# Optimization experiments

Hardware: AMD Instinct MI355X
Metric: run time of the kernel (lower is better)

The kernel has to match this reference:

```python
import jax, jax.numpy as jnp
import numpy as np

E = 100000          # number of edges
NS, NV = 128, 64    # scalar / vector multiplicities of node irreps (128x0e + 64x1e)
FC = 64             # radial MLP width (fc_neurons = [64, 64])
WN = NS + NS + NV + NV + NV   # depthwise-TP weight numel = 448
VOUT = 64           # gated vector channels after linear
EPS = 1e-5
SQRT3 = 3.0 ** 0.5
SQRT2 = 2.0 ** 0.5


def setup_inputs() -> dict:
    key = jax.random.key(0)
    ks = jax.random.split(key, 12)

    def n(k, shape, scale=1.0):
        return jax.random.normal(k, shape, dtype=jnp.float32) * scale

    return dict(
        node_input=n(ks[0], (E, NS + 3 * NV)),   # [E, 320] gathered node features
        edge_attr=n(ks[1], (E, 4)),              # [E, 1(0e) + 3(1e)] spherical harmonics
        edge_scalars=n(ks[2], (E, FC)),          # [E, 64] radial embedding
        # radial MLP (RadialProfile): 64 -> 64 -> 64 -> 448 (+ offset)
        W1=n(ks[3], (FC, FC), FC ** -0.5), b1=jnp.zeros((FC,), jnp.float32),
        W2=n(ks[4], (FC, FC), FC ** -0.5), b2=jnp.zeros((FC,), jnp.float32),
        W3=n(ks[5], (FC, WN), FC ** -0.5), offset=jnp.zeros((WN,), jnp.float32),
        # irrep-wise linear (LinearRS): scalars 192->192 (incl. gates), vectors 256->64
        Ws=n(ks[6], (NS + NV, NS + NV), (NS + NV) ** -0.5),
        bs=jnp.zeros((NS + NV,), jnp.float32),
        Wv=n(ks[7], (NS + 2 * NV, VOUT), (NS + 2 * NV) ** -0.5),
        # equivariant layer-norm affine params
        g_s=jnp.ones((NS + NV,), jnp.float32), b_n=jnp.zeros((NS + NV,), jnp.float32),
        g_v=jnp.ones((VOUT,), jnp.float32),
    )


def _forward(node_input, edge_attr, edge_scalars, W1, b1, W2, b2, W3, offset,
             Ws, bs, Wv, g_s, b_n, g_v):
    # --- radial MLP -> per-edge depthwise-TP weights (dtp_rad) ---
    h = jax.nn.silu(edge_scalars @ W1 + b1)
    h = jax.nn.silu(h @ W2 + b2)
    w = h @ W3 + offset                                   # [E, 448]
    w1 = w[:, :NS]                 # 0e x 0e -> 0e  (128)
    w2 = w[:, NS:2 * NS]           # 0e x 1e -> 1e  (128)
    w3 = w[:, 2 * NS:2 * NS + NV]  # 1e x 0e -> 1e  (64)
    w4 = w[:, 2 * NS + NV:2 * NS + 2 * NV]   # 1e x 1e -> 0e (64)
    w5 = w[:, 2 * NS + 2 * NV:]              # 1e x 1e -> 1e (64)

    s = node_input[:, :NS]                    # [E, 128] scalar block
    v = node_input[:, NS:].reshape(-1, NV, 3) # [E, 64, 3] vector block
    e0 = edge_attr[:, 0:1]                    # [E, 1]
    e1 = edge_attr[:, 1:4]                    # [E, 3]

    # --- depthwise tensor product (per-edge CG contractions, 'uvu') ---
    o0a = w1 * s * e0                                          # [E,128]
    o0b = w4 * (v * e1[:, None, :]).sum(-1) / SQRT3            # [E,64]
    o1a = (w2 * s)[:, :, None] * e1[:, None, :]                # [E,128,3]
    o1b = w3[:, :, None] * v * e0[:, :, None]                  # [E,64,3]
    o1c = w5[:, :, None] * jnp.cross(v, e1[:, None, :]) / SQRT2  # [E,64,3]

    scal = jnp.concatenate([o0a, o0b], axis=-1)                # [E,192]
    vec = jnp.concatenate([o1a, o1b, o1c], axis=1)             # [E,256,3]

    # --- irrep-wise linear mix ---
    s_lin = scal @ Ws + bs                                     # [E,192]
    v_lin = jnp.einsum('euc,uo->eoc', vec, Wv)                 # [E,64,3]

    # --- equivariant layer norm (component normalization per irrep block) ---
    s_c = s_lin - s_lin.mean(-1, keepdims=True)
    s_norm = jax.lax.rsqrt((s_c ** 2).mean(-1, keepdims=True) + EPS)
    s_n = g_s * s_c * s_norm + b_n
    v_norm = jax.lax.rsqrt((v_lin ** 2).sum(-1).mean(-1) + EPS)  # [E]
    v_n = g_v[:, None] * v_lin * v_norm[:, None, None]

    # --- gated activation: SiLU on scalars, sigmoid gates on vectors ---
    out_s = jax.nn.silu(s_n[:, :NS])                           # [E,128]
    gates = jax.nn.sigmoid(s_n[:, NS:])                        # [E,64]
    out_v = v_n * gates[:, :, None]                            # [E,64,3]
    return jnp.concatenate([out_s, out_v.reshape(-1, 3 * VOUT)], axis=-1)


def reference(node_input, edge_attr, edge_scalars, W1, b1, W2, b2, W3, offset,
              Ws, bs, Wv, g_s, b_n, g_v):
    return _forward(node_input, edge_attr, edge_scalars, W1, b1, W2, b2, W3, offset,
                    Ws, bs, Wv, g_s, b_n, g_v)
```

## Files before the change

### kernel.cpp

```cpp
#include <hip/hip_runtime.h>

typedef short short8 __attribute__((ext_vector_type(8)));
typedef __bf16 bf16x8 __attribute__((ext_vector_type(8)));
typedef float f32x4 __attribute__((ext_vector_type(4)));

namespace {

constexpr int kNodeW = 320;
constexpr int kOutW  = 320;

constexpr int F_W1 = 0;
constexpr int F_W2 = 8;
constexpr int F_W3 = 16;
constexpr int F_WS = 72;
constexpr int F_WP = 144;
constexpr int F_WQ = 160;
constexpr int F_WR = 168;
constexpr int NFRAG = 176;

constexpr int WAVES = 4;
constexpr int ARENA_OFF = 152 * 1024;
constexpr int SMEM_SZ = 160 * 1024;

constexpr float RS3 = 0.5773502691896258f;
constexpr float RS2 = 0.7071067811865476f;

__device__ __forceinline__ ushort f2b(float f) {
  __bf16 b = (__bf16)f;
  return __builtin_bit_cast(ushort, b);
}
__device__ __forceinline__ float fsig(float x) { return 1.0f / (1.0f + __expf(-x)); }
__device__ __forceinline__ float fsilu(float x) { return x / (1.0f + __expf(-x)); }
__device__ __forceinline__ f32x4 MFMA(short8 a, short8 b, f32x4 c) {
  return __builtin_amdgcn_mfma_f32_16x16x32_bf16(
      __builtin_bit_cast(bf16x8, a), __builtin_bit_cast(bf16x8, b), c, 0, 0, 0);
}

__device__ __forceinline__ void cw16(char* ar, int row, int col, ushort v) {
  *(ushort*)(ar + ((row * 128 + col * 2) ^ ((row & 7) << 4))) = v;
}
__device__ __forceinline__ short8 cra(const char* ar, int row, int kb, int lg) {
  return *(const short8*)(ar + ((row * 128 + kb * 64 + lg * 16) ^ ((row & 7) << 4)));
}

__global__ void pack_weights(const float* __restrict__ W1, const float* __restrict__ W2,
                             const float* __restrict__ W3, const float* __restrict__ Ws,
                             const float* __restrict__ Wv, ushort* __restrict__ dst) {
  int f = blockIdx.x, lane = threadIdx.x;
  const float* src; int ldw, kbase, NT, local;
  if (f < 8)        { src = W1; ldw = 64;  kbase = 0;   NT = 4;  local = f; }
  else if (f < 16)  { src = W2; ldw = 64;  kbase = 0;   NT = 4;  local = f - 8; }
  else if (f < 72)  { src = W3; ldw = 448; kbase = 0;   NT = 28; local = f - 16; }
  else if (f < 144) { src = Ws; ldw = 192; kbase = 0;   NT = 12; local = f - 72; }
  else if (f < 160) { src = Wv; ldw = 64;  kbase = 0;   NT = 4;  local = f - 144; }
  else if (f < 168) { src = Wv; ldw = 64;  kbase = 128; NT = 4;  local = f - 160; }
  else              { src = Wv; ldw = 64;  kbase = 192; NT = 4;  local = f - 168; }
  int kb = local / NT, nt = local % NT;
  int k0  = kbase + kb * 32 + (lane >> 4) * 8;
  int col = nt * 16 + (lane & 15);
  ushort* o = dst + ((size_t)f * 64 + lane) * 8;
#pragma unroll
  for (int j = 0; j < 8; ++j) o[j] = f2b(src[(size_t)(k0 + j) * ldw + col]);
}

__global__ __launch_bounds__(256, 1) void fctp_main(
    const float* __restrict__ node, const float* __restrict__ eattr,
    const float* __restrict__ es, const float* __restrict__ b1,
    const float* __restrict__ b2, const float* __restrict__ offs,
    const float* __restrict__ bs, const float* __restrict__ g_s,
    const float* __restrict__ b_n, const float* __restrict__ g_v,
    const short8* __restrict__ wsv, float* __restrict__ out, int E) {
  __shared__ __align__(16) char smem[SMEM_SZ];
  const int lane = threadIdx.x & 63, wave = threadIdx.x >> 6;
  const int l15 = lane & 15, lg = lane >> 4;

#pragma unroll
  for (int i = 0; i < 38; ++i) {
    int fl = wave * 38 + i;
    int fg = (fl < 56)  ? (F_W3 + fl)
           : (fl < 128) ? (F_WS + (fl - 56))
           : (fl < 136) ? (F_WQ + (fl - 128))
           : (fl < 144) ? (F_WR + (fl - 136))
                        : (F_WP + (fl - 144));
    *(short8*)(smem + fl * 1024 + lane * 16) = wsv[fg * 64 + lane];
  }
  __syncthreads();

  short8 w1f[8], w2f[8];
#pragma unroll
  for (int i = 0; i < 8; ++i) {
    w1f[i] = wsv[(F_W1 + i) * 64 + lane];
    w2f[i] = wsv[(F_W2 + i) * 64 + lane];
  }

  char* ar = smem + ARENA_OFF + wave * 2048;
  auto ldsB = [&](int f) -> short8 {
    return *(const short8*)(smem + f * 1024 + lane * 16);
  };

  const int ntiles = (E + 15) >> 4;
  for (int tile = (int)blockIdx.x * WAVES + wave; tile < ntiles;
       tile += (int)gridDim.x * WAVES) {
    const int e0 = tile * 16;
    int geA = e0 + l15; if (geA >= E) geA = E - 1;
    int geR[4];
    float e0v[4], e1v[4][3];
#pragma unroll
    for (int r = 0; r < 4; ++r) {
      int g = e0 + lg * 4 + r; if (g >= E) g = E - 1;
      geR[r] = g;
      float4 ea = *(const float4*)(eattr + (size_t)g * 4);
      e0v[r] = ea.x; e1v[r][0] = ea.y; e1v[r][1] = ea.z; e1v[r][2] = ea.w;
    }

    float sn[4][8];
    float vn[4][4][3];
#pragma unroll
    for (int r = 0; r < 4; ++r) {
      const float* ni = node + (size_t)geR[r] * kNodeW;
#pragma unroll
      for (int nt = 0; nt < 8; ++nt) sn[r][nt] = ni[nt * 16 + l15];
#pragma unroll
      for (int nt = 0; nt < 4; ++nt) {
        const float* vp = ni + 128 + 3 * (nt * 16 + l15);
        vn[r][nt][0] = vp[0]; vn[r][nt][1] = vp[1]; vn[r][nt][2] = vp[2];
      }
    }

    short8 aes[2];
#pragma unroll
    for (int kb = 0; kb < 2; ++kb) {
      const float* p = es + (size_t)geA * 64 + kb * 32 + lg * 8;
      float4 xa = *(const float4*)p, xb = *(const float4*)(p + 4);
      short8 a;
      a[0] = (short)f2b(xa.x); a[1] = (short)f2b(xa.y); a[2] = (short)f2b(xa.z); a[3] = (short)f2b(xa.w);
      a[4] = (short)f2b(xb.x); a[5] = (short)f2b(xb.y); a[6] = (short)f2b(xb.z); a[7] = (short)f2b(xb.w);
      aes[kb] = a;
    }

    short8 ah[2];
    {
      f32x4 acc[4];
#pragma unroll
      for (int nt = 0; nt < 4; ++nt) { float bv = b1[nt * 16 + l15]; acc[nt] = (f32x4){bv, bv, bv, bv}; }
      __builtin_amdgcn_s_setprio(1);
#pragma unroll
      for (int kb = 0; kb < 2; ++kb)
#pragma unroll
        for (int nt = 0; nt < 4; ++nt)
          acc[nt] = MFMA(aes[kb], w1f[kb * 4 + nt], acc[nt]);
      __builtin_amdgcn_s_setprio(0);
#pragma unroll
      for (int nt = 0; nt < 4; ++nt)
#pragma unroll
        for (int r = 0; r < 4; ++r)
          cw16(ar, lg * 4 + r, nt * 16 + l15, f2b(fsilu(acc[nt][r])));
      ah[0] = cra(ar, l15, 0, lg);
      ah[1] = cra(ar, l15, 1, lg);
    }
    {
      f32x4 acc[4];
#pragma unroll
      for (int nt = 0; nt < 4; ++nt) { float bv = b2[nt * 16 + l15]; acc[nt] = (f32x4){bv, bv, bv, bv}; }
      __builtin_amdgcn_s_setprio(1);
#pragma unroll
      for (int kb = 0; kb < 2; ++kb)
#pragma unroll
        for (int nt = 0; nt < 4; ++nt)
          acc[nt] = MFMA(ah[kb], w2f[kb * 4 + nt], acc[nt]);
      __builtin_amdgcn_s_setprio(0);
#pragma unroll
      for (int nt = 0; nt < 4; ++nt)
#pragma unroll
        for (int r = 0; r < 4; ++r)
          cw16(ar, lg * 4 + r, nt * 16 + l15, f2b(fsilu(acc[nt][r])));
      ah[0] = cra(ar, l15, 0, lg);
      ah[1] = cra(ar, l15, 1, lg);
    }

    auto wseg = [&](int seg, f32x4 (&w)[4]) {
#pragma unroll
      for (int nt = 0; nt < 4; ++nt) {
        float bv = offs[seg * 64 + nt * 16 + l15];
        w[nt] = (f32x4){bv, bv, bv, bv};
      }
      __builtin_amdgcn_s_setprio(1);
#pragma unroll
      for (int kb = 0; kb < 2; ++kb)
#pragma unroll
        for (int nt = 0; nt < 4; ++nt)
          w[nt] = MFMA(ah[kb], ldsB(kb * 28 + seg * 4 + nt), w[nt]);
      __builtin_amdgcn_s_setprio(0);
    };
    auto gemm12 = [&](int kb0, f32x4 (&sac)[12]) {
      short8 a0 = cra(ar, l15, 0, lg), a1 = cra(ar, l15, 1, lg);
      __builtin_amdgcn_s_setprio(1);
#pragma unroll
      for (int nt = 0; nt < 12; ++nt)
        sac[nt] = MFMA(a0, ldsB(56 + kb0 * 12 + nt), sac[nt]);
#pragma unroll
      for (int nt = 0; nt < 12; ++nt)
        sac[nt] = MFMA(a1, ldsB(56 + (kb0 + 1) * 12 + nt), sac[nt]);
      __builtin_amdgcn_s_setprio(0);
    };
    auto gemm4g = [&](int fb0, int fb1, f32x4 (&ac)[4]) {
      short8 a0 = cra(ar, l15, 0, lg), a1 = cra(ar, l15, 1, lg);
      __builtin_amdgcn_s_setprio(1);
#pragma unroll
      for (int nt = 0; nt < 4; ++nt) ac[nt] = MFMA(a0, wsv[(fb0 + nt) * 64 + lane], ac[nt]);
#pragma unroll
      for (int nt = 0; nt < 4; ++nt) ac[nt] = MFMA(a1, wsv[(fb1 + nt) * 64 + lane], ac[nt]);
      __builtin_amdgcn_s_setprio(0);
    };
    auto gemm4L = [&](int s0, f32x4 (&ac)[4]) {
      short8 a0 = cra(ar, l15, 0, lg), a1 = cra(ar, l15, 1, lg);
      __builtin_amdgcn_s_setprio(1);
#pragma unroll
      for (int nt = 0; nt < 4; ++nt) ac[nt] = MFMA(a0, ldsB(s0 + nt), ac[nt]);
#pragma unroll
      for (int nt = 0; nt < 4; ++nt) ac[nt] = MFMA(a1, ldsB(s0 + 4 + nt), ac[nt]);
      __builtin_amdgcn_s_setprio(0);
    };
    auto tpS = [&](const f32x4 (&w)[4], int nb, bool mulE0) {
#pragma unroll
      for (int nt = 0; nt < 4; ++nt)
#pragma unroll
        for (int r = 0; r < 4; ++r) {
          float v = w[nt][r] * sn[r][nb + nt];
          if (mulE0) v *= e0v[r];
          cw16(ar, lg * 4 + r, nt * 16 + l15, f2b(v));
        }
    };
    auto tpD = [&](const f32x4 (&w)[4]) {
#pragma unroll
      for (int nt = 0; nt < 4; ++nt)
#pragma unroll
        for (int r = 0; r < 4; ++r) {
          float dot = vn[r][nt][0] * e1v[r][0] + vn[r][nt][1] * e1v[r][1] +
                      vn[r][nt][2] * e1v[r][2];
          cw16(ar, lg * 4 + r, nt * 16 + l15, f2b(w[nt][r] * dot * RS3));
        }
    };
    auto tpQ = [&](const f32x4 (&w)[4], int c) {
#pragma unroll
      for (int nt = 0; nt < 4; ++nt)
#pragma unroll
        for (int r = 0; r < 4; ++r)
          cw16(ar, lg * 4 + r, nt * 16 + l15,
               f2b(e0v[r] * w[nt][r] * vn[r][nt][c]));
    };
    auto tpR = [&](const f32x4 (&w)[4], int c) {
      const int i1 = (c + 1) % 3, i2 = (c + 2) % 3;
#pragma unroll
      for (int nt = 0; nt < 4; ++nt)
#pragma unroll
        for (int r = 0; r < 4; ++r) {
          float cr = vn[r][nt][i1] * e1v[r][i2] - vn[r][nt][i2] * e1v[r][i1];
          cw16(ar, lg * 4 + r, nt * 16 + l15, f2b(w[nt][r] * cr * RS2));
        }
    };

    f32x4 wacc[4];
    f32x4 sacc[12];
#pragma unroll
    for (int nt = 0; nt < 12; ++nt) { float bv = bs[nt * 16 + l15]; sacc[nt] = (f32x4){bv, bv, bv, bv}; }
    wseg(0, wacc); tpS(wacc, 0, true);  gemm12(0, sacc);
    wseg(1, wacc); tpS(wacc, 4, true);  gemm12(2, sacc);
    wseg(5, wacc); tpD(wacc);           gemm12(4, sacc);

    float gate[4][4];
    {
      float gsv[12], bnv[12];
#pragma unroll
      for (int nt = 0; nt < 12; ++nt) { gsv[nt] = g_s[nt * 16 + l15]; bnv[nt] = b_n[nt * 16 + l15]; }
#pragma unroll
      for (int r = 0; r < 4; ++r) {
        float sx = 0.f, sxx = 0.f;
#pragma unroll
        for (int nt = 0; nt < 12; ++nt) { float v = sacc[nt][r]; sx += v; sxx += v * v; }
#pragma unroll
        for (int m = 8; m >= 1; m >>= 1) { sx += __shfl_xor(sx, m); sxx += __shfl_xor(sxx, m); }
        float mean = sx * (1.0f / 192.0f);
        float var  = sxx * (1.0f / 192.0f) - mean * mean;
        float rstd = rsqrtf(var + 1e-5f);
        int geu = e0 + lg * 4 + r;
        bool valid = geu < E;
        float* ob = out + (size_t)(valid ? geu : 0) * kOutW;
#pragma unroll
        for (int nt = 0; nt < 12; ++nt) {
          float s_n = gsv[nt] * (sacc[nt][r] - mean) * rstd + bnv[nt];
          if (nt < 8) { if (valid) ob[nt * 16 + l15] = fsilu(s_n); }
          else gate[r][nt - 8] = fsig(s_n);
        }
      }
    }

    f32x4 pacc[4];
#pragma unroll
    for (int nt = 0; nt < 4; ++nt) pacc[nt] = (f32x4){0.f, 0.f, 0.f, 0.f};
    wseg(2, wacc); tpS(wacc, 0, false); gemm4L(144, pacc);
    wseg(3, wacc); tpS(wacc, 4, false); gemm4g(F_WP + 8, F_WP + 12, pacc);

    f32x4 vl[3][4];
    wseg(4, wacc);
#pragma unroll
    for (int c = 0; c < 3; ++c) {
#pragma unroll
      for (int nt = 0; nt < 4; ++nt)
#pragma unroll
        for (int r = 0; r < 4; ++r)
          vl[c][nt][r] = pacc[nt][r] * e1v[r][c];
      tpQ(wacc, c);
      gemm4L(128, vl[c]);
    }
    wseg(6, wacc);
#pragma unroll
    for (int c = 0; c < 3; ++c) {
      tpR(wacc, c);
      gemm4L(136, vl[c]);
    }

    {
      float gvv[4];
#pragma unroll
      for (int nt = 0; nt < 4; ++nt) gvv[nt] = g_v[nt * 16 + l15];
#pragma unroll
      for (int r = 0; r < 4; ++r) {
        float vsq = 0.f;
#pragma unroll
        for (int c = 0; c < 3; ++c)
#pragma unroll
          for (int nt = 0; nt < 4; ++nt) { float v = vl[c][nt][r]; vsq += v * v; }
#pragma unroll
        for (int m = 8; m >= 1; m >>= 1) vsq += __shfl_xor(vsq, m);
        float vnrm = rsqrtf(vsq * (1.0f / 64.0f) + 1e-5f);
        int geu = e0 + lg * 4 + r;
        if (geu < E) {
          float* ob = out + (size_t)geu * kOutW + 128;
#pragma unroll
          for (int nt = 0; nt < 4; ++nt) {
            float m3 = gvv[nt] * vnrm * gate[r][nt];
            int o3 = (nt * 16 + l15) * 3;
            ob[o3 + 0] = m3 * vl[0][nt][r];
            ob[o3 + 1] = m3 * vl[1][nt][r];
            ob[o3 + 2] = m3 * vl[2][nt][r];
          }
        }
      }
    }
  }
}

}

extern "C" void kernel_launch(void* const* d_in, const int* in_sizes, int n_in,
                              void* d_out, int out_size, void* d_ws, size_t ws_size,
                              hipStream_t stream) {
  const float* node_input   = (const float*)d_in[0];
  const float* edge_attr    = (const float*)d_in[1];
  const float* edge_scalars = (const float*)d_in[2];
  const float* W1 = (const float*)d_in[3];
  const float* b1 = (const float*)d_in[4];
  const float* W2 = (const float*)d_in[5];
  const float* b2 = (const float*)d_in[6];
  const float* W3 = (const float*)d_in[7];
  const float* offset = (const float*)d_in[8];
  const float* Ws = (const float*)d_in[9];
  const float* bs = (const float*)d_in[10];
  const float* Wv = (const float*)d_in[11];
  const float* g_s = (const float*)d_in[12];
  const float* b_n = (const float*)d_in[13];
  const float* g_v = (const float*)d_in[14];
  float* out = (float*)d_out;

  const int E = in_sizes[0] / kNodeW;

  pack_weights<<<NFRAG, 64, 0, stream>>>(W1, W2, W3, Ws, Wv, (ushort*)d_ws);

  const int ntiles = (E + 15) / 16;
  int blocks = (ntiles + WAVES - 1) / WAVES;
  if (blocks > 256) blocks = 256;
  fctp_main<<<blocks, WAVES * 64, 0, stream>>>(
      node_input, edge_attr, edge_scalars, b1, b2, offset, bs, g_s, b_n, g_v,
      (const short8*)d_ws, out, E);
}
```

Measured before the change: 180.0 us.

## Software-pipeline per-tile global loads with double-buffered register state

Restructures the persistent tile loop so each wave prefetches the next tile's edge attributes, scalar node features, edge scalars and vector node features into a second register state while the current tile's GEMMs run. The loop is unrolled by two and alternates between two EState buffers. The aim is to hide global-memory latency behind MFMA work. In exchange it roughly doubles the per-thread register footprint for input state, which risks spills or lower occupancy. Prefetch addresses past the end are clamped to E-1, so those reads stay in bounds.

```diff
diff --git a/kernel.cpp b/kernel.cpp
--- a/kernel.cpp
+++ b/kernel.cpp
@@ -42,6 +42,15 @@
 __device__ __forceinline__ short8 cra(const char* ar, int row, int kb, int lg) {
   return *(const short8*)(ar + ((row * 128 + kb * 64 + lg * 16) ^ ((row & 7) << 4)));
 }
+
+struct EState {
+  int   geR[4];
+  float e0v[4];
+  float e1v[4][3];
+  float sn[4][8];
+  float vn[4][4][3];
+  float4 esr[4];
+};
 
 __global__ void pack_weights(const float* __restrict__ W1, const float* __restrict__ W2,
                              const float* __restrict__ W3, const float* __restrict__ Ws,
@@ -99,39 +108,52 @@
   };
 
   const int ntiles = (E + 15) >> 4;
-  for (int tile = (int)blockIdx.x * WAVES + wave; tile < ntiles;
-       tile += (int)gridDim.x * WAVES) {
-    const int e0 = tile * 16;
+  const int stride = (int)gridDim.x * WAVES;
+  int tl0 = (int)blockIdx.x * WAVES + wave;
+  if (tl0 >= ntiles) return;
+
+  auto loadHead = [&](int tl, EState& S) {
+    const int e0 = tl * 16;
     int geA = e0 + l15; if (geA >= E) geA = E - 1;
-    int geR[4];
-    float e0v[4], e1v[4][3];
 #pragma unroll
     for (int r = 0; r < 4; ++r) {
       int g = e0 + lg * 4 + r; if (g >= E) g = E - 1;
-      geR[r] = g;
+      S.geR[r] = g;
       float4 ea = *(const float4*)(eattr + (size_t)g * 4);
-      e0v[r] = ea.x; e1v[r][0] = ea.y; e1v[r][1] = ea.z; e1v[r][2] = ea.w;
-    }
-
-    float sn[4][8];
-    float vn[4][4][3];
+      S.e0v[r] = ea.x; S.e1v[r][0] = ea.y; S.e1v[r][1] = ea.z; S.e1v[r][2] = ea.w;
+    }
 #pragma unroll
     for (int r = 0; r < 4; ++r) {
-      const float* ni = node + (size_t)geR[r] * kNodeW;
-#pragma unroll
-      for (int nt = 0; nt < 8; ++nt) sn[r][nt] = ni[nt * 16 + l15];
+      const float* ni = node + (size_t)S.geR[r] * kNodeW;
+#pragma unroll
+      for (int nt = 0; nt < 8; ++nt) S.sn[r][nt] = ni[nt * 16 + l15];
+    }
+#pragma unroll
+    for (int kb = 0; kb < 2; ++kb) {
+      const float* p = es + (size_t)geA * 64 + kb * 32 + lg * 8;
+      S.esr[kb * 2]     = *(const float4*)p;
+      S.esr[kb * 2 + 1] = *(const float4*)(p + 4);
+    }
+  };
+  auto loadVn = [&](EState& S) {
+#pragma unroll
+    for (int r = 0; r < 4; ++r) {
+      const float* ni = node + (size_t)S.geR[r] * kNodeW;
 #pragma unroll
       for (int nt = 0; nt < 4; ++nt) {
         const float* vp = ni + 128 + 3 * (nt * 16 + l15);
-        vn[r][nt][0] = vp[0]; vn[r][nt][1] = vp[1]; vn[r][nt][2] = vp[2];
+        S.vn[r][nt][0] = vp[0]; S.vn[r][nt][1] = vp[1]; S.vn[r][nt][2] = vp[2];
       }
     }
+  };
+
+  auto body = [&](int tl, EState& C, EState& N) {
+    const int e0 = tl * 16;
 
     short8 aes[2];
 #pragma unroll
     for (int kb = 0; kb < 2; ++kb) {
-      const float* p = es + (size_t)geA * 64 + kb * 32 + lg * 8;
-      float4 xa = *(const float4*)p, xb = *(const float4*)(p + 4);
+      float4 xa = C.esr[kb * 2], xb = C.esr[kb * 2 + 1];
       short8 a;
       a[0] = (short)f2b(xa.x); a[1] = (short)f2b(xa.y); a[2] = (short)f2b(xa.z); a[3] = (short)f2b(xa.w);
       a[4] = (short)f2b(xb.x); a[5] = (short)f2b(xb.y); a[6] = (short)f2b(xb.z); a[7] = (short)f2b(xb.w);
@@ -226,8 +248,8 @@
       for (int nt = 0; nt < 4; ++nt)
 #pragma unroll
         for (int r = 0; r < 4; ++r) {
-          float v = w[nt][r] * sn[r][nb + nt];
-          if (mulE0) v *= e0v[r];
+          float v = w[nt][r] * C.sn[r][nb + nt];
+          if (mulE0) v *= C.e0v[r];
           cw16(ar, lg * 4 + r, nt * 16 + l15, f2b(v));
         }
     };
@@ -236,8 +258,8 @@
       for (int nt = 0; nt < 4; ++nt)
 #pragma unroll
         for (int r = 0; r < 4; ++r) {
-          float dot = vn[r][nt][0] * e1v[r][0] + vn[r][nt][1] * e1v[r][1] +
-                      vn[r][nt][2] * e1v[r][2];
+          float dot = C.vn[r][nt][0] * C.e1v[r][0] + C.vn[r][nt][1] * C.e1v[r][1] +
+                      C.vn[r][nt][2] * C.e1v[r][2];
           cw16(ar, lg * 4 + r, nt * 16 + l15, f2b(w[nt][r] * dot * RS3));
         }
     };
@@ -247,7 +269,7 @@
 #pragma unroll
         for (int r = 0; r < 4; ++r)
           cw16(ar, lg * 4 + r, nt * 16 + l15,
-               f2b(e0v[r] * w[nt][r] * vn[r][nt][c]));
+               f2b(C.e0v[r] * w[nt][r] * C.vn[r][nt][c]));
     };
     auto tpR = [&](const f32x4 (&w)[4], int c) {
       const int i1 = (c + 1) % 3, i2 = (c + 2) % 3;
@@ -255,7 +277,7 @@
       for (int nt = 0; nt < 4; ++nt)
 #pragma unroll
         for (int r = 0; r < 4; ++r) {
-          float cr = vn[r][nt][i1] * e1v[r][i2] - vn[r][nt][i2] * e1v[r][i1];
+          float cr = C.vn[r][nt][i1] * C.e1v[r][i2] - C.vn[r][nt][i2] * C.e1v[r][i1];
           cw16(ar, lg * 4 + r, nt * 16 + l15, f2b(w[nt][r] * cr * RS2));
         }
     };
@@ -301,6 +323,8 @@
     wseg(2, wacc); tpS(wacc, 0, false); gemm4L(144, pacc);
     wseg(3, wacc); tpS(wacc, 4, false); gemm4g(F_WP + 8, F_WP + 12, pacc);
 
+    loadHead(tl + stride, N);
+
     f32x4 vl[3][4];
     wseg(4, wacc);
 #pragma unroll
@@ -309,7 +333,7 @@
       for (int nt = 0; nt < 4; ++nt)
 #pragma unroll
         for (int r = 0; r < 4; ++r)
-          vl[c][nt][r] = pacc[nt][r] * e1v[r][c];
+          vl[c][nt][r] = pacc[nt][r] * C.e1v[r][c];
       tpQ(wacc, c);
       gemm4L(128, vl[c]);
     }
@@ -319,6 +343,8 @@
       tpR(wacc, c);
       gemm4L(136, vl[c]);
     }
+
+    loadVn(N);
 
     {
       float gvv[4];
@@ -348,6 +374,17 @@
         }
       }
     }
+  };
+
+  EState S0, S1;
+  loadHead(tl0, S0);
+  loadVn(S0);
+  int tl = tl0;
+  for (;;) {
+    body(tl, S0, S1);
+    tl += stride; if (tl >= ntiles) break;
+    body(tl, S1, S0);
+    tl += stride; if (tl >= ntiles) break;
   }
 }
 
```

Result: slower. 221.0 us (+22.8%).
